# Optimization experiments

Hardware: AMD Instinct MI355X
Metric: run time of the kernel (lower is better)

The kernel has to match this reference:

```python
import jax, jax.numpy as jnp
import numpy as np

N_NODES = 100000
N_EDGES = 1600000


def _glorot(key, shape):
    lim = float(np.sqrt(6.0 / (shape[0] + shape[1])))
    return jax.random.uniform(key, shape, jnp.float32, -lim, lim)


def setup_inputs() -> dict:
    key = jax.random.key(0)
    ks = jax.random.split(key, 12)
    x = jax.random.normal(ks[0], (N_NODES, 8), jnp.float32)
    edge_index = jax.random.randint(ks[1], (2, N_EDGES), 0, N_NODES, jnp.int64)
    dims = [(8, 32), (32, 32), (32, 32), (32, 32), (32, 3)]
    params = {}
    for i, (din, dout) in enumerate(dims):
        params[f"W{i+1}"] = _glorot(ks[2 + i], (din, dout))
        params[f"b{i+1}"] = jnp.zeros((dout,), jnp.float32)
    return {"x": x, "edge_index": edge_index, **params}


def _gcn_norm(edge_index, num_nodes):
    # add self-loops, symmetric normalization (PyG GCNConv defaults)
    loops = jnp.arange(num_nodes, dtype=edge_index.dtype)
    row = jnp.concatenate([edge_index[0], loops])
    col = jnp.concatenate([edge_index[1], loops])
    deg = jax.ops.segment_sum(jnp.ones_like(col, jnp.float32), col,
                              num_segments=num_nodes)
    dinv = jnp.where(deg > 0, jax.lax.rsqrt(deg), 0.0)
    norm = dinv[row] * dinv[col]  # [E + N]
    return row, col, norm


def _gcn_conv(h, W, b, row, col, norm, num_nodes):
    h = h @ W                                   # [N, dout]
    msg = h[row] * norm[:, None]                # gather + scale
    out = jax.ops.segment_sum(msg, col, num_segments=num_nodes)
    return out + b


def reference(x, edge_index, W1, b1, W2, b2, W3, b3, W4, b4, W5, b5):
    row, col, norm = _gcn_norm(edge_index, N_NODES)
    lrelu = lambda h: jax.nn.leaky_relu(h, negative_slope=1.0)  # identity, kept faithful
    h = lrelu(_gcn_conv(x, W1, b1, row, col, norm, N_NODES))
    h = lrelu(_gcn_conv(h, W2, b2, row, col, norm, N_NODES))
    h = lrelu(_gcn_conv(h, W3, b3, row, col, norm, N_NODES))
    h = lrelu(_gcn_conv(h, W4, b4, row, col, norm, N_NODES))
    h = lrelu(_gcn_conv(h, W5, b5, row, col, norm, N_NODES))
    return h
```

## Files before the change

### kernel.cpp

```cpp
#include <hip/hip_runtime.h>

#define NN 100000
#define NE 1600000
#define NB 391
#define EPB 3125
#define NBLK 512
#define CAP 5632
#define RCAP 4608



__global__ __launch_bounds__(512) void bucket_scatter_kernel(const void* __restrict__ ei,
                                                             int* __restrict__ bcursor,
                                                             unsigned int* __restrict__ epacked) {
    __shared__ int lcount[NB];
    __shared__ int lcur[NB];
    int tid = threadIdx.x;
    for (int i = tid; i < NB; i += 512) lcount[i] = 0;
    int base = blockIdx.x * EPB;
    unsigned int hw = ((const unsigned int*)ei)[2 * (base + tid) + 1];
    int is64 = (__ballot(hw != 0) == 0ULL);
    int r[7], c[7];
    r[6] = -1;
    if (!is64) {
        const int* e32 = (const int*)ei;
#pragma unroll
        for (int k = 0; k < 6; k++) {
            int e = base + k * 512 + tid;
            r[k] = e32[e];
            c[k] = e32[NE + e];
        }
        if (tid < EPB - 6 * 512) {
            int e = base + 6 * 512 + tid;
            r[6] = e32[e];
            c[6] = e32[NE + e];
        }
    } else {
        const long long* e64 = (const long long*)ei;
#pragma unroll
        for (int k = 0; k < 6; k++) {
            int e = base + k * 512 + tid;
            r[k] = (int)e64[e];
            c[k] = (int)e64[(long long)NE + e];
        }
        if (tid < EPB - 6 * 512) {
            int e = base + 6 * 512 + tid;
            r[6] = (int)e64[e];
            c[6] = (int)e64[(long long)NE + e];
        }
    }
    __syncthreads();
#pragma unroll
    for (int k = 0; k < 7; k++)
        if (r[k] >= 0) atomicAdd(&lcount[c[k] >> 8], 1);
    __syncthreads();
    for (int i = tid; i < NB; i += 512) {
        int cnt = lcount[i];
        lcur[i] = (cnt ? atomicAdd(&bcursor[i], cnt) : 0) + i * CAP;
    }
    __syncthreads();
#pragma unroll
    for (int k = 0; k < 7; k++) {
        if (r[k] >= 0) {
            int b = c[k] >> 8;
            int pos = atomicAdd(&lcur[b], 1);
            if (pos < b * CAP + RCAP)
                epacked[pos] = ((unsigned)(c[k] & 255) << 24) | (unsigned)r[k];
        }
    }
}


__global__ __launch_bounds__(512) void bucket_csr_kernel(
    const unsigned int* __restrict__ epacked, const int* __restrict__ bcount,
    const float* __restrict__ x,
    const float* __restrict__ W1, const float* __restrict__ b1,
    const float* __restrict__ W2, const float* __restrict__ b2,
    const float* __restrict__ W3, const float* __restrict__ b3,
    const float* __restrict__ W4, const float* __restrict__ b4,
    const float* __restrict__ W5, const float* __restrict__ b5,
    float* __restrict__ cv,
    int2* __restrict__ meta, int* __restrict__ srow,
    float4* __restrict__ Ta, float4* __restrict__ Tb, int N) {
    __shared__ float w45[96], w345[96], w2345[96];
    __shared__ float4 Wl4[8];
    __shared__ int lcount[256];
    __shared__ int lcur[256];
    __shared__ int wsum[4];
    __shared__ int ptot;
    __shared__ int sbuf[CAP];
    int b = blockIdx.x;
    int tid = threadIdx.x;
    int s0 = b * CAP;
    int cnt = bcount[b];
    if (cnt > RCAP) cnt = RCAP;
    if (tid < 256) lcount[tid] = 0;
    for (int i = tid; i < CAP; i += 512) sbuf[i] = NN;
    int i3 = tid / 3, j3 = tid - 3 * (tid / 3);
    if (tid < 96) {
        float s = 0.0f;
        for (int k = 0; k < 32; k++) s += W4[i3 * 32 + k] * W5[k * 3 + j3];
        w45[i3 * 3 + j3] = s;
    }
    __syncthreads();
    unsigned int ev[9];
#pragma unroll
    for (int k = 0; k < 9; k++) {
        int i = k * 512 + tid;
        ev[k] = (i < cnt) ? epacked[s0 + i] : 0xFFFFFFFFu;
    }
    if (tid < 96) {
        float s = 0.0f;
        for (int k = 0; k < 32; k++) s += W3[i3 * 32 + k] * w45[k * 3 + j3];
        w345[i3 * 3 + j3] = s;
    }
    __syncthreads();
    if (tid < 96) {
        float s = 0.0f;
        for (int k = 0; k < 32; k++) s += W2[i3 * 32 + k] * w345[k * 3 + j3];
        w2345[i3 * 3 + j3] = s;
    }
    __syncthreads();
    if (tid < 32) {
        int ii = tid >> 2, jj = tid & 3;
        float s = 0.0f;
        if (jj < 3)
            for (int k = 0; k < 32; k++) s += W1[ii * 32 + k] * w2345[k * 3 + jj];
        ((float*)Wl4)[tid] = s;
    }
    if (b == 0 && tid >= 32 && tid < 52) {
        int kk = (tid - 32) >> 2, jj = (tid - 32) & 3;
        float s = 0.0f;
        if (jj < 3) {
            if (kk == 0) for (int k = 0; k < 32; k++) s += b1[k] * w2345[k * 3 + jj];
            if (kk == 1) for (int k = 0; k < 32; k++) s += b2[k] * w345[k * 3 + jj];
            if (kk == 2) for (int k = 0; k < 32; k++) s += b3[k] * w45[k * 3 + jj];
            if (kk == 3) for (int k = 0; k < 32; k++) s += b4[k] * W5[k * 3 + jj];
            if (kk == 4) s = b5[jj];
        }
        cv[tid - 32] = s;
    }
    if (b == 0 && tid == 52) {
        Ta[NN] = make_float4(0.f, 0.f, 0.f, 0.f);
        Tb[NN] = make_float4(0.f, 0.f, 0.f, 0.f);
    }
#pragma unroll
    for (int k = 0; k < 9; k++)
        if (ev[k] != 0xFFFFFFFFu) atomicAdd(&lcount[ev[k] >> 24], 1);
    __syncthreads();
    int lane = tid & 63, w = tid >> 6;
    int myc = (tid < 256) ? lcount[tid] : 0;
    int myp = (myc + 3) & ~3;
    int acc = myp;
#pragma unroll
    for (int off = 1; off < 64; off <<= 1) {
        int y = __shfl_up(acc, off);
        if (lane >= off) acc += y;
    }
    if (lane == 63 && w < 4) wsum[w] = acc;
    __syncthreads();
    if (tid == 0) {
        int s = 0;
#pragma unroll
        for (int j = 0; j < 4; j++) { int t = wsum[j]; wsum[j] = s; s += t; }
    }
    __syncthreads();
    if (tid < 256) {
        int excl = acc - myp + wsum[w];
        lcur[tid] = excl;
        if (tid == 255) ptot = excl + myp;
        int col = (b << 8) + tid;
        if (col < N) {
            meta[col] = make_int2(s0 + excl, myc);
            float d = 1.0f / sqrtf((float)myc + 1.0f);
            const float4* x4 = (const float4*)x + col * 2;
            float4 av = x4[0], bv = x4[1];
            float xs[8] = {av.x, av.y, av.z, av.w, bv.x, bv.y, bv.z, bv.w};
            float4 o = make_float4(0.f, 0.f, 0.f, 0.f);
#pragma unroll
            for (int k = 0; k < 8; k++) {
                float4 ww = Wl4[k];
                o.x += xs[k] * ww.x; o.y += xs[k] * ww.y; o.z += xs[k] * ww.z;
            }
            o.x *= d; o.y *= d; o.z *= d; o.w = 0.0f;
            Ta[col] = o;
        }
    }
    __syncthreads();
#pragma unroll
    for (int k = 0; k < 9; k++) {
        if (ev[k] != 0xFFFFFFFFu) {
            int p = atomicAdd(&lcur[ev[k] >> 24], 1);
            sbuf[p] = (int)(ev[k] & 0xFFFFFFu);
        }
    }
    __syncthreads();
    int pt = ptot;
    for (int i = tid; i < pt; i += 512) srow[s0 + i] = sbuf[i];
}


template <bool LAST>
__global__ __launch_bounds__(256) void prop_kernel(
    const int2* __restrict__ meta, const int* __restrict__ srow,
    const float4* __restrict__ tin, const float* __restrict__ cv, int k,
    float4* __restrict__ tout, float* __restrict__ out, int N) {
    int tid = blockIdx.x * 256 + threadIdx.x;
    int c = tid >> 2, q = tid & 3;
    if (c >= N) return;
    int2 m = meta[c];
    int s = m.x;
    int d = m.y;
    int dpad = (d + 3) & ~3;
    float ax = 0.f, ay = 0.f, az = 0.f;
    if (q == 0) { float4 t = tin[c]; ax = t.x; ay = t.y; az = t.z; }
    float bx = 0.f, by = 0.f, bz = 0.f;
    float cx = 0.f, cy = 0.f, cz = 0.f;
    float dx = 0.f, dy = 0.f, dz = 0.f;
    for (int j = 4 * q; j < dpad; j += 16) {
        int4 rr = *(const int4*)(srow + s + j);
        float4 v0 = tin[rr.x];
        float4 v1 = tin[rr.y];
        float4 v2 = tin[rr.z];
        float4 v3 = tin[rr.w];
        ax += v0.x; ay += v0.y; az += v0.z;
        bx += v1.x; by += v1.y; bz += v1.z;
        cx += v2.x; cy += v2.y; cz += v2.z;
        dx += v3.x; dy += v3.y; dz += v3.z;
    }
    ax += bx + cx + dx;
    ay += by + cy + dy;
    az += bz + cz + dz;
    ax += __shfl_xor(ax, 1); ay += __shfl_xor(ay, 1); az += __shfl_xor(az, 1);
    ax += __shfl_xor(ax, 2); ay += __shfl_xor(ay, 2); az += __shfl_xor(az, 2);
    if (q == 0) {
        float dd = 1.0f / sqrtf((float)d + 1.0f);
        float vx = cv[k * 4 + 0], vy = cv[k * 4 + 1], vz = cv[k * 4 + 2];
        if (LAST) {
            out[c * 3 + 0] = dd * ax + vx;
            out[c * 3 + 1] = dd * ay + vy;
            out[c * 3 + 2] = dd * az + vz;
        } else {
            float d2 = dd * dd;
            float4 o;
            o.x = d2 * ax + dd * vx;
            o.y = d2 * ay + dd * vy;
            o.z = d2 * az + dd * vz;
            o.w = 0.0f;
            tout[c] = o;
        }
    }
}


extern "C" void kernel_launch(void* const* d_in, const int* in_sizes, int n_in,
                              void* d_out, int out_size, void* d_ws, size_t ws_size,
                              hipStream_t stream) {
    const float* x  = (const float*)d_in[0];
    const void*  ei = d_in[1];
    const float* W1 = (const float*)d_in[2];  const float* b1 = (const float*)d_in[3];
    const float* W2 = (const float*)d_in[4];  const float* b2 = (const float*)d_in[5];
    const float* W3 = (const float*)d_in[6];  const float* b3 = (const float*)d_in[7];
    const float* W4 = (const float*)d_in[8];  const float* b4 = (const float*)d_in[9];
    const float* W5 = (const float*)d_in[10]; const float* b5 = (const float*)d_in[11];
    float* out = (float*)d_out;

    char* p = (char*)d_ws;
    auto alloc = [&](size_t bytes) {
        char* r = p;
        p += (bytes + 255) & ~(size_t)255;
        return r;
    };
    int2*  meta    = (int2*)alloc((size_t)NN * 8);
    int*   bcursor = (int*)alloc(NB * 4);
    float* cv      = (float*)alloc(5 * 4 * 4);
    unsigned int* epacked = (unsigned int*)alloc((size_t)NB * CAP * 4);
    int*          srow    = (int*)alloc((size_t)NB * CAP * 4);
    float4*       Ta      = (float4*)alloc((size_t)(NN + 1) * 16);
    float4*       Tb      = (float4*)alloc((size_t)(NN + 1) * 16);
    if ((size_t)(p - (char*)d_ws) > ws_size) return;

    hipMemsetAsync(bcursor, 0, NB * 4, stream);
    bucket_scatter_kernel<<<NBLK, 512, 0, stream>>>(ei, bcursor, epacked);
    bucket_csr_kernel<<<NB, 512, 0, stream>>>(epacked, bcursor, x,
                                              W1, b1, W2, b2, W3, b3, W4, b4, W5, b5,
                                              cv, meta, srow, Ta, Tb, NN);

    int gP = (NN * 4 + 255) / 256;
    prop_kernel<false><<<gP, 256, 0, stream>>>(meta, srow, Ta, cv, 0, Tb, nullptr, NN);
    prop_kernel<false><<<gP, 256, 0, stream>>>(meta, srow, Tb, cv, 1, Ta, nullptr, NN);
    prop_kernel<false><<<gP, 256, 0, stream>>>(meta, srow, Ta, cv, 2, Tb, nullptr, NN);
    prop_kernel<false><<<gP, 256, 0, stream>>>(meta, srow, Tb, cv, 3, Ta, nullptr, NN);
    prop_kernel<true><<<gP, 256, 0, stream>>>(meta, srow, Ta, cv, 4, nullptr, out, NN);
}
```

Measured before the change: 171.0 us.

## Replace global atomic bucket cursors with per-block sorted slots and transposed count tables

The scatter kernel now sorts its edges by bucket in shared memory and writes them contiguously to a global slot array, along with per-block count and start tables stored bucket-major. This removes the global atomic cursors and the memset. The CSR kernel prefix-sums those tables and gathers each bucket's segments from all 512 source blocks. That makes the output deterministic and the writes coalesced, but each thread in the CSR kernel now does a short serial read of scattered segments. Separately, the propagation kernels move from 256 to 512 threads per block.

```diff
diff --git a/kernel.cpp b/kernel.cpp
--- a/kernel.cpp
+++ b/kernel.cpp
@@ -11,10 +11,14 @@
 
 
 __global__ __launch_bounds__(512) void bucket_scatter_kernel(const void* __restrict__ ei,
-                                                             int* __restrict__ bcursor,
-                                                             unsigned int* __restrict__ epacked) {
+                                                             unsigned int* __restrict__ gslot,
+                                                             int* __restrict__ cntT,
+                                                             int* __restrict__ startT) {
     __shared__ int lcount[NB];
+    __shared__ int lstart[NB];
     __shared__ int lcur[NB];
+    __shared__ int wsum[8];
+    __shared__ unsigned int slotv[EPB];
     int tid = threadIdx.x;
     for (int i = tid; i < NB; i += 512) lcount[i] = 0;
     int base = blockIdx.x * EPB;
@@ -54,25 +58,48 @@
     for (int k = 0; k < 7; k++)
         if (r[k] >= 0) atomicAdd(&lcount[c[k] >> 8], 1);
     __syncthreads();
-    for (int i = tid; i < NB; i += 512) {
-        int cnt = lcount[i];
-        lcur[i] = (cnt ? atomicAdd(&bcursor[i], cnt) : 0) + i * CAP;
+    int lane = tid & 63, w = tid >> 6;
+    int v = (tid < NB) ? lcount[tid] : 0;
+    int acc = v;
+#pragma unroll
+    for (int off = 1; off < 64; off <<= 1) {
+        int y = __shfl_up(acc, off);
+        if (lane >= off) acc += y;
+    }
+    if (lane == 63) wsum[w] = acc;
+    __syncthreads();
+    if (tid == 0) {
+        int s = 0;
+#pragma unroll
+        for (int j = 0; j < 8; j++) { int t = wsum[j]; wsum[j] = s; s += t; }
+    }
+    __syncthreads();
+    acc += wsum[w];
+    if (tid < NB) {
+        int excl = acc - v;
+        lstart[tid] = excl;
+        lcur[tid] = excl;
     }
     __syncthreads();
 #pragma unroll
     for (int k = 0; k < 7; k++) {
         if (r[k] >= 0) {
-            int b = c[k] >> 8;
-            int pos = atomicAdd(&lcur[b], 1);
-            if (pos < b * CAP + RCAP)
-                epacked[pos] = ((unsigned)(c[k] & 255) << 24) | (unsigned)r[k];
-        }
+            int pos = atomicAdd(&lcur[c[k] >> 8], 1);
+            slotv[pos] = ((unsigned)(c[k] & 255) << 24) | (unsigned)r[k];
+        }
+    }
+    __syncthreads();
+    for (int i = tid; i < EPB; i += 512) gslot[base + i] = slotv[i];
+    for (int i = tid; i < NB; i += 512) {
+        cntT[i * NBLK + blockIdx.x] = lcount[i];
+        startT[i * NBLK + blockIdx.x] = lstart[i];
     }
 }
 
 
 __global__ __launch_bounds__(512) void bucket_csr_kernel(
-    const unsigned int* __restrict__ epacked, const int* __restrict__ bcount,
+    const unsigned int* __restrict__ gslot,
+    const int* __restrict__ cntT, const int* __restrict__ startT,
     const float* __restrict__ x,
     const float* __restrict__ W1, const float* __restrict__ b1,
     const float* __restrict__ W2, const float* __restrict__ b2,
@@ -86,16 +113,40 @@
     __shared__ float4 Wl4[8];
     __shared__ int lcount[256];
     __shared__ int lcur[256];
-    __shared__ int wsum[4];
-    __shared__ int ptot;
-    __shared__ int sbuf[CAP];
+    __shared__ int wsum[8];
+    __shared__ int stot, ptot;
+    __shared__ unsigned int sbufraw[RCAP];
+    __shared__ int sbuf2[CAP];
     int b = blockIdx.x;
     int tid = threadIdx.x;
     int s0 = b * CAP;
-    int cnt = bcount[b];
-    if (cnt > RCAP) cnt = RCAP;
     if (tid < 256) lcount[tid] = 0;
-    for (int i = tid; i < CAP; i += 512) sbuf[i] = NN;
+    for (int i = tid; i < CAP; i += 512) sbuf2[i] = NN;
+    int rc = cntT[b * NBLK + tid];
+    int rs = startT[b * NBLK + tid];
+    int lane = tid & 63, w = tid >> 6;
+    int acc = rc;
+#pragma unroll
+    for (int off = 1; off < 64; off <<= 1) {
+        int y = __shfl_up(acc, off);
+        if (lane >= off) acc += y;
+    }
+    if (lane == 63) wsum[w] = acc;
+    __syncthreads();
+    if (tid == 0) {
+        int s = 0;
+#pragma unroll
+        for (int j = 0; j < 8; j++) { int t = wsum[j]; wsum[j] = s; s += t; }
+    }
+    __syncthreads();
+    acc += wsum[w];
+    int roff = acc - rc;
+    if (tid == 511) stot = roff + rc;
+    const unsigned int* src = gslot + (size_t)tid * EPB + rs;
+    for (int j = 0; j < rc; j++) {
+        int p = roff + j;
+        if (p < RCAP) sbufraw[p] = src[j];
+    }
     int i3 = tid / 3, j3 = tid - 3 * (tid / 3);
     if (tid < 96) {
         float s = 0.0f;
@@ -103,12 +154,6 @@
         w45[i3 * 3 + j3] = s;
     }
     __syncthreads();
-    unsigned int ev[9];
-#pragma unroll
-    for (int k = 0; k < 9; k++) {
-        int i = k * 512 + tid;
-        ev[k] = (i < cnt) ? epacked[s0 + i] : 0xFFFFFFFFu;
-    }
     if (tid < 96) {
         float s = 0.0f;
         for (int k = 0; k < 32; k++) s += W3[i3 * 32 + k] * w45[k * 3 + j3];
@@ -144,14 +189,15 @@
         Ta[NN] = make_float4(0.f, 0.f, 0.f, 0.f);
         Tb[NN] = make_float4(0.f, 0.f, 0.f, 0.f);
     }
-#pragma unroll
-    for (int k = 0; k < 9; k++)
-        if (ev[k] != 0xFFFFFFFFu) atomicAdd(&lcount[ev[k] >> 24], 1);
-    __syncthreads();
-    int lane = tid & 63, w = tid >> 6;
+    __syncthreads();
+    int cnt = stot;
+    if (cnt > RCAP) cnt = RCAP;
+    for (int i = tid; i < cnt; i += 512)
+        atomicAdd(&lcount[sbufraw[i] >> 24], 1);
+    __syncthreads();
     int myc = (tid < 256) ? lcount[tid] : 0;
     int myp = (myc + 3) & ~3;
-    int acc = myp;
+    acc = myp;
 #pragma unroll
     for (int off = 1; off < 64; off <<= 1) {
         int y = __shfl_up(acc, off);
@@ -187,25 +233,23 @@
         }
     }
     __syncthreads();
-#pragma unroll
-    for (int k = 0; k < 9; k++) {
-        if (ev[k] != 0xFFFFFFFFu) {
-            int p = atomicAdd(&lcur[ev[k] >> 24], 1);
-            sbuf[p] = (int)(ev[k] & 0xFFFFFFu);
-        }
+    for (int i = tid; i < cnt; i += 512) {
+        unsigned int vv = sbufraw[i];
+        int p = atomicAdd(&lcur[vv >> 24], 1);
+        sbuf2[p] = (int)(vv & 0xFFFFFFu);
     }
     __syncthreads();
     int pt = ptot;
-    for (int i = tid; i < pt; i += 512) srow[s0 + i] = sbuf[i];
+    for (int i = tid; i < pt; i += 512) srow[s0 + i] = sbuf2[i];
 }
 
 
 template <bool LAST>
-__global__ __launch_bounds__(256) void prop_kernel(
+__global__ __launch_bounds__(512) void prop_kernel(
     const int2* __restrict__ meta, const int* __restrict__ srow,
     const float4* __restrict__ tin, const float* __restrict__ cv, int k,
     float4* __restrict__ tout, float* __restrict__ out, int N) {
-    int tid = blockIdx.x * 256 + threadIdx.x;
+    int tid = blockIdx.x * 512 + threadIdx.x;
     int c = tid >> 2, q = tid & 3;
     if (c >= N) return;
     int2 m = meta[c];
@@ -272,24 +316,24 @@
         return r;
     };
     int2*  meta    = (int2*)alloc((size_t)NN * 8);
-    int*   bcursor = (int*)alloc(NB * 4);
     float* cv      = (float*)alloc(5 * 4 * 4);
-    unsigned int* epacked = (unsigned int*)alloc((size_t)NB * CAP * 4);
-    int*          srow    = (int*)alloc((size_t)NB * CAP * 4);
-    float4*       Ta      = (float4*)alloc((size_t)(NN + 1) * 16);
-    float4*       Tb      = (float4*)alloc((size_t)(NN + 1) * 16);
+    unsigned int* gslot = (unsigned int*)alloc((size_t)NE * 4);
+    int*   cntT    = (int*)alloc((size_t)NB * NBLK * 4);
+    int*   startT  = (int*)alloc((size_t)NB * NBLK * 4);
+    int*   srow    = (int*)alloc((size_t)NB * CAP * 4);
+    float4* Ta     = (float4*)alloc((size_t)(NN + 1) * 16);
+    float4* Tb     = (float4*)alloc((size_t)(NN + 1) * 16);
     if ((size_t)(p - (char*)d_ws) > ws_size) return;
 
-    hipMemsetAsync(bcursor, 0, NB * 4, stream);
-    bucket_scatter_kernel<<<NBLK, 512, 0, stream>>>(ei, bcursor, epacked);
-    bucket_csr_kernel<<<NB, 512, 0, stream>>>(epacked, bcursor, x,
+    bucket_scatter_kernel<<<NBLK, 512, 0, stream>>>(ei, gslot, cntT, startT);
+    bucket_csr_kernel<<<NB, 512, 0, stream>>>(gslot, cntT, startT, x,
                                               W1, b1, W2, b2, W3, b3, W4, b4, W5, b5,
                                               cv, meta, srow, Ta, Tb, NN);
 
-    int gP = (NN * 4 + 255) / 256;
-    prop_kernel<false><<<gP, 256, 0, stream>>>(meta, srow, Ta, cv, 0, Tb, nullptr, NN);
-    prop_kernel<false><<<gP, 256, 0, stream>>>(meta, srow, Tb, cv, 1, Ta, nullptr, NN);
-    prop_kernel<false><<<gP, 256, 0, stream>>>(meta, srow, Ta, cv, 2, Tb, nullptr, NN);
-    prop_kernel<false><<<gP, 256, 0, stream>>>(meta, srow, Tb, cv, 3, Ta, nullptr, NN);
-    prop_kernel<true><<<gP, 256, 0, stream>>>(meta, srow, Ta, cv, 4, nullptr, out, NN);
+    int gP = (NN * 4 + 511) / 512;
+    prop_kernel<false><<<gP, 512, 0, stream>>>(meta, srow, Ta, cv, 0, Tb, nullptr, NN);
+    prop_kernel<false><<<gP, 512, 0, stream>>>(meta, srow, Tb, cv, 1, Ta, nullptr, NN);
+    prop_kernel<false><<<gP, 512, 0, stream>>>(meta, srow, Ta, cv, 2, Tb, nullptr, NN);
+    prop_kernel<false><<<gP, 512, 0, stream>>>(meta, srow, Tb, cv, 3, Ta, nullptr, NN);
+    prop_kernel<true><<<gP, 512, 0, stream>>>(meta, srow, Ta, cv, 4, nullptr, out, NN);
 }
```

Result: no change. 170.6 us (-0.3%).
